# Optimization experiments

Hardware: AMD Instinct MI355X
Metric: run time of the kernel (lower is better)

## Reference

```python
import jax, jax.numpy as jnp
import numpy as np
import math

D_K = 64

def setup_inputs() -> dict:
    key = jax.random.key(0)
    ks = jax.random.split(key, 7)
    B, S, d = 8, 2048, D_K
    H = 4096
    Q = jax.random.normal(ks[0], (B, S, d), dtype=jnp.float32)
    K = jax.random.normal(ks[1], (B, S, d), dtype=jnp.float32)
    V = jax.random.normal(ks[2], (B, S, d), dtype=jnp.float32)
    # Linear params (stored as [in, out]); scaled like torch default init
    W1 = jax.random.normal(ks[3], (S, H), dtype=jnp.float32) / math.sqrt(S)
    b1 = jnp.zeros((H,), dtype=jnp.float32)
    W2 = jax.random.normal(ks[4], (H, S), dtype=jnp.float32) / math.sqrt(H)
    b2 = jnp.zeros((S,), dtype=jnp.float32)
    return {"Q": Q, "K": K, "V": V, "W1": W1, "b1": b1, "W2": W2, "b2": b2}

def reference(Q, K, V, W1, b1, W2, b2):
    # scores: [B, Sq, Sk]
    scores = jnp.einsum('bqd,bkd->bqk', Q, K) / jnp.sqrt(jnp.float32(D_K))
    # 2-layer MLP applied along the last (Sk) axis of the scores
    h = jax.nn.relu(jnp.einsum('bqk,kh->bqh', scores, W1) + b1)
    adjusted = jnp.einsum('bqh,hk->bqk', h, W2) + b2
    attn = jax.nn.softmax(adjusted, axis=-1)
    return jnp.einsum('bqk,bkd->bqd', attn, V)
```

## Files before the change

kernel.cpp:

```cpp
#include <hip/hip_runtime.h>
#include <hip/hip_bf16.h>
#include <stdint.h>

#define S 2048
#define D 64
#define H 4096
#define NB 8

typedef __bf16 bf16;
typedef __attribute__((ext_vector_type(8))) __bf16 bf16x8;
typedef __attribute__((ext_vector_type(4))) __bf16 bf16x4;
typedef __attribute__((ext_vector_type(4))) float f32x4;

__device__ __forceinline__ void dma16_raw(const bf16* g, uint32_t m0_bytes) {
  uint32_t m0s = __builtin_amdgcn_readfirstlane(m0_bytes);
  asm volatile("s_mov_b32 m0, %1\n\t"
               "global_load_lds_dwordx4 %0, off"
               :: "v"(g), "s"(m0s) : "memory");
}

__device__ __forceinline__ uint32_t lds_off_bytes(const void* p) {
  return (uint32_t)(uintptr_t)(__attribute__((address_space(3))) const void*)p;
}

__global__ __launch_bounds__(256) void mega_prep(
    const float* __restrict__ W1, bf16* __restrict__ W1t,
    const float* __restrict__ W2, bf16* __restrict__ W2t,
    const float* __restrict__ Q, bf16* __restrict__ Qb,
    const float* __restrict__ Km, bf16* __restrict__ Kb,
    const float* __restrict__ V, bf16* __restrict__ VtAll) {
  __shared__ float tile[64][65];
  int b = blockIdx.x;
  int tid = threadIdx.x;
  int c4 = (tid & 15) * 4;
  int r16 = tid >> 4;

  if (b < 4096) {
    const float* W; bf16* Wt; int K, N, x, y;
    if (b < 2048) { W = W1; Wt = W1t; K = S; N = H; x = b & 63; y = b >> 6; }
    else { int t = b - 2048; W = W2; Wt = W2t; K = H; N = S; x = t & 31; y = t >> 5; }
    int k0 = y * 64, n0 = x * 64;
#pragma unroll
    for (int i = 0; i < 4; ++i) {
      int r = i * 16 + r16;
      f32x4 v = *(const f32x4*)&W[(size_t)(k0 + r) * N + n0 + c4];
      tile[r][c4 + 0] = v.x; tile[r][c4 + 1] = v.y;
      tile[r][c4 + 2] = v.z; tile[r][c4 + 3] = v.w;
    }
    __syncthreads();
#pragma unroll
    for (int i = 0; i < 4; ++i) {
      int n = i * 16 + r16;
      bf16x4 o;
      o[0] = (bf16)tile[c4 + 0][n]; o[1] = (bf16)tile[c4 + 1][n];
      o[2] = (bf16)tile[c4 + 2][n]; o[3] = (bf16)tile[c4 + 3][n];
      *(bf16x4*)&Wt[(size_t)(n0 + n) * K + k0 + c4] = o;
    }
  } else if (b < 6144) {
    int t = b - 4096;
    const float* x = (t >> 10) ? Km : Q;
    bf16* y = (t >> 10) ? Kb : Qb;
    int i = (t & 1023) * 256 + tid;
    f32x4 v = ((const f32x4*)x)[i];
    bf16x4 o;
    o[0] = (bf16)v.x; o[1] = (bf16)v.y; o[2] = (bf16)v.z; o[3] = (bf16)v.w;
    ((bf16x4*)y)[i] = o;
  } else {
    int t = b - 6144;
    int s0 = (t & 31) * 64;
    int z = t >> 5;
    const float* Vb = V + (size_t)z * (S * D);
    bf16* Vtb = VtAll + (size_t)z * (D * S);
#pragma unroll
    for (int i = 0; i < 4; ++i) {
      int r = i * 16 + r16;
      f32x4 v = *(const f32x4*)&Vb[(size_t)(s0 + r) * D + c4];
      tile[r][c4 + 0] = v.x; tile[r][c4 + 1] = v.y;
      tile[r][c4 + 2] = v.z; tile[r][c4 + 3] = v.w;
    }
    __syncthreads();
#pragma unroll
    for (int i = 0; i < 4; ++i) {
      int n = i * 16 + r16;
      bf16x4 o;
      o[0] = (bf16)tile[c4 + 0][n]; o[1] = (bf16)tile[c4 + 1][n];
      o[2] = (bf16)tile[c4 + 2][n]; o[3] = (bf16)tile[c4 + 3][n];
      *(bf16x4*)&Vtb[(size_t)n * S + s0 + c4] = o;
    }
  }
}

__global__ __launch_bounds__(256) void vt_cast(const float* __restrict__ V,
                                               bf16* __restrict__ Vt) {
  __shared__ float tile[64][65];
  int z = blockIdx.y;
  int s0 = blockIdx.x * 64;
  const float* Vb = V + (size_t)z * (S * D);
  bf16* Vtb = Vt + (size_t)z * (D * S);
  int c4 = (threadIdx.x & 15) * 4;
  int r16 = threadIdx.x >> 4;
#pragma unroll
  for (int i = 0; i < 4; ++i) {
    int r = i * 16 + r16;
    f32x4 v = *(const f32x4*)&Vb[(size_t)(s0 + r) * D + c4];
    tile[r][c4 + 0] = v.x; tile[r][c4 + 1] = v.y;
    tile[r][c4 + 2] = v.z; tile[r][c4 + 3] = v.w;
  }
  __syncthreads();
#pragma unroll
  for (int i = 0; i < 4; ++i) {
    int n = i * 16 + r16;
    bf16x4 o;
    o[0] = (bf16)tile[c4 + 0][n]; o[1] = (bf16)tile[c4 + 1][n];
    o[2] = (bf16)tile[c4 + 2][n]; o[3] = (bf16)tile[c4 + 3][n];
    *(bf16x4*)&Vtb[(size_t)n * S + s0 + c4] = o;
  }
}

__global__ __launch_bounds__(256, 2) void qk_bt(const bf16* __restrict__ Qb,
                                                const bf16* __restrict__ Kb,
                                                bf16* __restrict__ Sc) {
  __shared__ __align__(16) bf16 smem[24576];
  int tid = threadIdx.x;
  int lane = tid & 63;
  int w = tid >> 6;

  int m0 = blockIdx.y * 128, n0 = blockIdx.x * 256;
  const bf16* Ab = Qb + (size_t)blockIdx.z * (S * D);
  const bf16* Btb = Kb + (size_t)blockIdx.z * (S * D);

  int grow = tid >> 2;
  int gcol = (((lane & 3) ^ ((lane >> 3) & 3)) * 8);
  const bf16* gA0 = Ab + (size_t)(m0 + grow) * D + gcol;
  const bf16* gA1 = gA0 + (size_t)64 * D;
  const bf16* gB0 = Btb + (size_t)(n0 + grow) * D + gcol;
  const bf16* gB1 = gB0 + (size_t)64 * D;
  const bf16* gB2 = gB0 + (size_t)128 * D;
  const bf16* gB3 = gB0 + (size_t)192 * D;

  uint32_t ldsBase = lds_off_bytes(&smem[0]);
  uint32_t wb = (uint32_t)(w * 1024);
  uint32_t mA[2], mB[2];
  mA[0] = ldsBase + wb;          mA[1] = ldsBase + 8192 + wb;
  mB[0] = ldsBase + 16384 + wb;  mB[1] = ldsBase + 32768 + wb;

  int mw = (w & 1) * 64, nw = (w >> 1) * 128;
  int lr = lane & 15;
  int ck = lane >> 4;
  int swz = (ck ^ ((lr >> 1) & 3)) * 8;
  const bf16* paBase = smem + (size_t)(mw + lr) * 32 + swz;
  const bf16* pbBase = smem + 8192 + (size_t)(nw + lr) * 32 + swz;

  f32x4 zero = {0.f, 0.f, 0.f, 0.f};
  f32x4 acc[4][8];
#pragma unroll
  for (int mt = 0; mt < 4; ++mt)
#pragma unroll
    for (int nt = 0; nt < 8; ++nt) acc[mt][nt] = zero;

#define STAGE(buf, koff)                                 \
  do {                                                   \
    dma16_raw(gA0 + (koff), mA[buf]);                    \
    dma16_raw(gA1 + (koff), mA[buf] + 4096);             \
    dma16_raw(gB0 + (koff), mB[buf]);                    \
    dma16_raw(gB1 + (koff), mB[buf] + 4096);             \
    dma16_raw(gB2 + (koff), mB[buf] + 8192);             \
    dma16_raw(gB3 + (koff), mB[buf] + 12288);            \
  } while (0)

  STAGE(0, 0);
  STAGE(1, 32);
#undef STAGE

#pragma unroll
  for (int it = 0; it < 2; ++it) {
    if (it == 0)
      asm volatile("s_waitcnt vmcnt(6)\n\ts_barrier" ::: "memory");
    else
      asm volatile("s_waitcnt vmcnt(0)\n\ts_barrier" ::: "memory");
    const bf16* pa = paBase + it * 4096;
    const bf16* pb = pbBase + it * 8192;
    bf16x8 af[4], bfr[8];
#pragma unroll
    for (int mt = 0; mt < 4; ++mt) af[mt] = *(const bf16x8*)(pa + mt * (16 * 32));
#pragma unroll
    for (int nt = 0; nt < 8; ++nt) bfr[nt] = *(const bf16x8*)(pb + nt * (16 * 32));
#pragma unroll
    for (int mt = 0; mt < 4; ++mt)
#pragma unroll
      for (int nt = 0; nt < 8; ++nt)
        acc[mt][nt] = __builtin_amdgcn_mfma_f32_16x16x32_bf16(af[mt], bfr[nt],
                                                              acc[mt][nt], 0, 0, 0);
  }

  bf16* C = Sc + (size_t)blockIdx.z * (S * S);
  int mbase = m0 + mw + (lane >> 4) * 4;
  int nbase = n0 + nw + (lane & 15);
#pragma unroll
  for (int mt = 0; mt < 4; ++mt) {
#pragma unroll
    for (int nt = 0; nt < 8; ++nt) {
      int n = nbase + nt * 16;
#pragma unroll
      for (int reg = 0; reg < 4; ++reg) {
        int m = mbase + mt * 16 + reg;
        C[(size_t)m * S + n] = (bf16)(acc[mt][nt][reg] * 0.125f);
      }
    }
  }
}

template <int RELU, int OUTBF16>
__global__ __launch_bounds__(512, 2) void gemm256(const bf16* __restrict__ A,
                                                  const bf16* __restrict__ Bt,
                                                  const float* __restrict__ bias,
                                                  void* __restrict__ Cv,
                                                  float scale,
                                                  int M, int N, int K,
                                                  long strideA, long strideB,
                                                  long strideC) {
  __shared__ __align__(16) bf16 smem[65536];
  const char* smc = (const char*)&smem[0];

  int tid = threadIdx.x;
  int lane = tid & 63;
  int w = tid >> 6;
  int wm = w >> 2, wn = w & 3;

  unsigned gx = gridDim.x;
  unsigned nwg = gx * gridDim.y;
  unsigned flat = blockIdx.y * gx + blockIdx.x;
  unsigned q = nwg >> 3, r = nwg & 7, xcd = flat & 7, idx = flat >> 3;
  unsigned wg = (xcd < r ? xcd * (q + 1) : r * (q + 1) + (xcd - r) * q) + idx;
  int n0 = (int)(wg % gx) * 256;
  int m0 = (int)(wg / gx) * 256;

  const bf16* Ab = A + (size_t)blockIdx.z * strideA;
  const bf16* Btb = Bt + (size_t)blockIdx.z * strideB;

  int trow = tid >> 3;
  int tg = (tid & 7) ^ (trow & 7);
  const bf16* pgA = Ab + (size_t)(m0 + trow) * K + tg * 8;
  const bf16* pgB = Btb + (size_t)(n0 + trow) * K + tg * 8;
  const size_t s64K = (size_t)K * 64;

  uint32_t ldsBase = lds_off_bytes(&smem[0]);
  uint32_t mb = ldsBase + (uint32_t)(w * 1024);

  int j = lane >> 4, b2 = (lane >> 2) & 1;
  uint32_t rbA0 = (uint32_t)(wm * 8192 + (lane & 15) * 128 +
                             ((j ^ (lane & 3)) * 16) + b2 * 64);
  uint32_t rbA1 = rbA0 ^ 64u;
  uint32_t rbB0 = (uint32_t)(65536 + wn * 4096 + (lane & 15) * 128 +
                             ((j ^ (lane & 3)) * 16) + b2 * 64);
  uint32_t rbB1 = rbB0 ^ 64u;

  f32x4 acc[8][4];
#pragma unroll
  for (int a = 0; a < 8; ++a)
#pragma unroll
    for (int b = 0; b < 2 * 2; ++b) acc[a][b] = (f32x4){0.f, 0.f, 0.f, 0.f};

  bf16x8 af[4][2];
  bf16x8 bf0[2][2];
  bf16x8 bf1[2][2];

#define STG_A(PI, HH, LL, KC) \
  dma16_raw(pgA + (size_t)(2 * (HH) + (LL)) * s64K + (KC), \
            mb + (PI) * 32768 + (HH) * 16384 + (LL) * 8192)
#define STG_B(PI, HH, LL, KC) \
  dma16_raw(pgB + (size_t)(2 * (HH) + (LL)) * s64K + (KC), \
            mb + 65536 + (PI) * 32768 + (HH) * 16384 + (LL) * 8192)
#define STAGE_AH(PI, HH, KC) do { STG_A(PI, HH, 0, KC); STG_A(PI, HH, 1, KC); } while (0)
#define STAGE_BH(PI, HH, KC) do { STG_B(PI, HH, 0, KC); STG_B(PI, HH, 1, KC); } while (0)

#define RDA(PI, QA)                                                            \
  do {                                                                        \
    _Pragma("unroll") for (int mt = 0; mt < 4; ++mt) {                        \
      af[mt][0] = *(const bf16x8*)(smc + rbA0 + ((PI) * 32768 + (QA) * 16384 + mt * 2048)); \
      af[mt][1] = *(const bf16x8*)(smc + rbA1 + ((PI) * 32768 + (QA) * 16384 + mt * 2048)); \
    }                                                                         \
  } while (0)
#define RDB(PI, QB, BF)                                                        \
  do {                                                                        \
    _Pragma("unroll") for (int nt = 0; nt < 2; ++nt) {                        \
      BF[nt][0] = *(const bf16x8*)(smc + rbB0 + ((PI) * 32768 + (QB) * 16384 + nt * 2048)); \
      BF[nt][1] = *(const bf16x8*)(smc + rbB1 + ((PI) * 32768 + (QB) * 16384 + nt * 2048)); \
    }                                                                         \
  } while (0)

#define MFMA_Q(QA, QB, BF)                                                     \
  do {                                                                        \
    __builtin_amdgcn_s_setprio(1);                                            \
    _Pragma("unroll") for (int mt = 0; mt < 4; ++mt)                          \
      _Pragma("unroll") for (int nt = 0; nt < 2; ++nt) {                      \
        f32x4 c = acc[(QA) * 4 + mt][(QB) * 2 + nt];                          \
        c = __builtin_amdgcn_mfma_f32_16x16x32_bf16(af[mt][0], BF[nt][0], c, 0, 0, 0); \
        c = __builtin_amdgcn_mfma_f32_16x16x32_bf16(af[mt][1], BF[nt][1], c, 0, 0, 0); \
        acc[(QA) * 4 + mt][(QB) * 2 + nt] = c;                                \
      }                                                                       \
    __builtin_amdgcn_s_setprio(0);                                            \
  } while (0)

#define BAR() asm volatile("s_barrier" ::: "memory")
#define VMC4() asm volatile("s_waitcnt vmcnt(4)" ::: "memory")

#define TILE2(PI, TT)                                              \
  do {                                                             \
    int c1 = ((TT) + 1 < NT ? (TT) + 1 : NT - 1) * 64;             \
    int c2 = ((TT) + 2 < NT ? (TT) + 2 : NT - 1) * 64;             \
    MFMA_Q(0, 0, bf0);                                             \
    RDB(PI, 1, bf1);                                               \
    STAGE_BH((PI) ^ 1, 0, c1);                                     \
    BAR();                                                         \
    MFMA_Q(0, 1, bf1);                                             \
    RDA(PI, 1);                                                    \
    STAGE_AH(PI, 0, c2);                                           \
    BAR();                                                         \
    STAGE_BH(PI, 1, c2);                                           \
    MFMA_Q(1, 1, bf1);                                             \
    VMC4();                                                        \
    BAR();                                                         \
    MFMA_Q(1, 0, bf0);                                             \
    if ((TT) + 1 < NT) {                                           \
      RDA((PI) ^ 1, 0);                                            \
      RDB((PI) ^ 1, 0, bf0);                                       \
      STAGE_AH(PI, 1, c2);                                         \
      BAR();                                                       \
    }                                                              \
  } while (0)

  STAGE_AH(0, 0, 0);
  STAGE_BH(0, 1, 0);
  STAGE_AH(0, 1, 0);
  STAGE_BH(0, 0, 0);
  STAGE_AH(1, 0, 64);
  STAGE_BH(1, 1, 64);
  asm volatile("s_waitcnt vmcnt(4)\n\ts_barrier" ::: "memory");

  const int NT = K / 64;

  RDA(0, 0);
  RDB(0, 0, bf0);
  STAGE_AH(1, 1, 64);
  BAR();

  for (int T = 0; T < NT; T += 2) {
    TILE2(0, T);
    TILE2(1, T + 1);
  }
#undef TILE2
#undef VMC4
#undef BAR
#undef MFMA_Q
#undef RDB
#undef RDA
#undef STAGE_BH
#undef STAGE_AH
#undef STG_B
#undef STG_A

  asm volatile("s_waitcnt vmcnt(0)" ::: "memory");

  int rowb = m0 + wm * 64 + ((lane >> 4) << 2);
  int colb = n0 + wn * 32 + (lane & 15);
#pragma unroll
  for (int fn = 0; fn < 4; ++fn) {
    int n = colb + (fn >> 1) * 128 + (fn & 1) * 16;
    float bv = bias ? bias[n] : 0.f;
#pragma unroll
    for (int fm = 0; fm < 8; ++fm) {
      int mrow = rowb + (fm >> 2) * 128 + (fm & 3) * 16;
#pragma unroll
      for (int reg = 0; reg < 4; ++reg) {
        float v = acc[fm][fn][reg] * scale + bv;
        if (RELU) v = fmaxf(v, 0.f);
        int m = mrow + reg;
        if (OUTBF16) {
          bf16* C = (bf16*)Cv + (size_t)blockIdx.z * strideC;
          C[(size_t)m * N + n] = (bf16)v;
        } else {
          float* C = (float*)Cv + (size_t)blockIdx.z * strideC;
          C[(size_t)m * N + n] = v;
        }
      }
    }
  }
}

__global__ __launch_bounds__(256) void smav(const float* __restrict__ adj,
                                            const bf16* __restrict__ Vt,
                                            float* __restrict__ out,
                                            long adjStride) {
  int z = blockIdx.y;
  const float* adjb = adj + (size_t)z * adjStride;
  const bf16* Vtb = Vt + (size_t)z * (D * S);
  float* outb = out + (size_t)z * (S * D);
  int q0 = blockIdx.x * 16;
  __shared__ __align__(16) bf16 P[16 * 2048];
  __shared__ float rsum[16];
  int tid = threadIdx.x, w = tid >> 6, lane = tid & 63;
  char* Pc = (char*)&P[0];

#pragma unroll
  for (int i = 0; i < 4; ++i) {
    int r = w * 4 + i;
    const float* rowp = adjb + (size_t)(q0 + r) * S + lane * 4;
    f32x4 rv[8];
    float lm = -1e30f;
#pragma unroll
    for (int kk = 0; kk < 8; ++kk) {
      rv[kk] = *(const f32x4*)(rowp + kk * 256);
      lm = fmaxf(lm, fmaxf(fmaxf(rv[kk].x, rv[kk].y), fmaxf(rv[kk].z, rv[kk].w)));
    }
#pragma unroll
    for (int off = 32; off > 0; off >>= 1) lm = fmaxf(lm, __shfl_xor(lm, off));
    float s = 0.f;
    uint32_t wbase = (uint32_t)(r * 4096 + (lane & 1) * 8);
#pragma unroll
    for (int kk = 0; kk < 8; ++kk) {
      bf16x4 pb;
      pb[0] = (bf16)__expf(rv[kk].x - lm);
      pb[1] = (bf16)__expf(rv[kk].y - lm);
      pb[2] = (bf16)__expf(rv[kk].z - lm);
      pb[3] = (bf16)__expf(rv[kk].w - lm);
      s += (float)pb[0] + (float)pb[1] + (float)pb[2] + (float)pb[3];
      uint32_t g = (uint32_t)(lane >> 1) + (uint32_t)(kk * 32);
      uint32_t gs = g ^ (uint32_t)(r & 7);
      *(bf16x4*)(Pc + wbase + gs * 16) = pb;
    }
#pragma unroll
    for (int off = 32; off > 0; off >>= 1) s += __shfl_xor(s, off);
    if (lane == 0) rsum[r] = s;
  }
  __syncthreads();

  int dl = (w << 4) + (lane & 15);
  const bf16* vrow = Vtb + (size_t)dl * S + (lane >> 4) * 8;
  uint32_t rl = (uint32_t)(lane & 15);
  uint32_t abase = rl * 4096;
  uint32_t rx = rl & 7;
  f32x4 acc0 = {0.f, 0.f, 0.f, 0.f}, acc1 = {0.f, 0.f, 0.f, 0.f};
#pragma unroll 4
  for (int k0 = 0; k0 < S; k0 += 64) {
    uint32_t g0 = (uint32_t)(k0 >> 3) + (uint32_t)(lane >> 4);
    bf16x8 a0 = *(const bf16x8*)(Pc + abase + ((g0 ^ rx) * 16));
    bf16x8 b0 = *(const bf16x8*)(vrow + k0);
    acc0 = __builtin_amdgcn_mfma_f32_16x16x32_bf16(a0, b0, acc0, 0, 0, 0);
    uint32_t g1 = g0 + 4;
    bf16x8 a1 = *(const bf16x8*)(Pc + abase + ((g1 ^ rx) * 16));
    bf16x8 b1 = *(const bf16x8*)(vrow + k0 + 32);
    acc1 = __builtin_amdgcn_mfma_f32_16x16x32_bf16(a1, b1, acc1, 0, 0, 0);
  }
  f32x4 accs = acc0 + acc1;
#pragma unroll
  for (int reg = 0; reg < 4; ++reg) {
    int m = ((lane >> 4) << 2) + reg;
    outb[(size_t)(q0 + m) * D + dl] = accs[reg] / rsum[m];
  }
}

extern "C" void kernel_launch(void* const* d_in, const int* in_sizes, int n_in,
                              void* d_out, int out_size, void* d_ws, size_t ws_size,
                              hipStream_t stream) {
  const float* Q  = (const float*)d_in[0];
  const float* Km = (const float*)d_in[1];
  const float* V  = (const float*)d_in[2];
  const float* W1 = (const float*)d_in[3];
  const float* b1 = (const float*)d_in[4];
  const float* W2 = (const float*)d_in[5];
  const float* b2 = (const float*)d_in[6];
  float* out = (float*)d_out;
  char* ws = (char*)d_ws;

  bf16* W1t  = (bf16*)ws;
  bf16* W2t  = (bf16*)(ws + 16777216);
  bf16* Qb16 = (bf16*)(ws + 33554432);
  bf16* Kb16 = (bf16*)(ws + 35651584);

  int G = 1;
  if (ws_size >= 306184192ULL) G = 8;
  else if (ws_size >= 171966464ULL) G = 4;
  else if (ws_size >= 104857600ULL) G = 2;

  bf16* Sc   = (bf16*)(ws + 37748736);
  float* adj = (float*)(ws + 37748736);
  bf16* h    = (bf16*)(ws + 37748736 + (size_t)G * 16777216);

  size_t vtOff = 37748736ULL + (size_t)G * 33554432ULL;
  bf16* VtAll = nullptr;
  if (ws_size >= vtOff + 2097152ULL) VtAll = (bf16*)(ws + vtOff);

  int prepBlocks = VtAll ? (6144 + NB * 32) : 6144;
  mega_prep<<<dim3(prepBlocks), 256, 0, stream>>>(
      W1, W1t, W2, W2t, Q, Qb16, Km, Kb16, V, VtAll ? VtAll : W1t);

  for (int b0 = 0; b0 < NB; b0 += G) {
    qk_bt<<<dim3(S / 256, S / 128, G), 256, 0, stream>>>(
        Qb16 + (size_t)b0 * S * D, Kb16 + (size_t)b0 * S * D, Sc);
    gemm256<1, 1><<<dim3(H / 256, S / 256, G), 512, 0, stream>>>(
        Sc, W1t, b1, h, 1.0f, S, H, S, (long)S * S, 0L, (long)S * H);
    gemm256<0, 0><<<dim3(S / 256, S / 256, G), 512, 0, stream>>>(
        h, W2t, b2, adj, 1.0f, S, S, H, (long)S * H, 0L, (long)S * S);
    const bf16* VtBase;
    if (VtAll) {
      VtBase = VtAll + (size_t)b0 * D * S;
    } else {
      vt_cast<<<dim3(S / 64, G), 256, 0, stream>>>(V + (size_t)b0 * S * D, h);
      VtBase = h;
    }
    smav<<<dim3(S / 16, G), 256, 0, stream>>>(
        adj, VtBase, out + (size_t)b0 * S * D, (long)S * S);
  }
}
```

Measured before the change: 634.2 us.

## Fuse next group's QK^T into softmax-AV kernel to overlap stages

```diff
diff --git a/kernel.cpp b/kernel.cpp
--- a/kernel.cpp
+++ b/kernel.cpp
@@ -117,17 +117,15 @@
   }
 }
 
-__global__ __launch_bounds__(256, 2) void qk_bt(const bf16* __restrict__ Qb,
-                                                const bf16* __restrict__ Kb,
-                                                bf16* __restrict__ Sc) {
-  __shared__ __align__(16) bf16 smem[24576];
+__device__ __forceinline__ void qk_body(char* smc, const bf16* Ab,
+                                        const bf16* Btb, bf16* C,
+                                        int bx, int by) {
+  bf16* smem = (bf16*)smc;
   int tid = threadIdx.x;
   int lane = tid & 63;
   int w = tid >> 6;
 
-  int m0 = blockIdx.y * 128, n0 = blockIdx.x * 256;
-  const bf16* Ab = Qb + (size_t)blockIdx.z * (S * D);
-  const bf16* Btb = Kb + (size_t)blockIdx.z * (S * D);
+  int m0 = by * 128, n0 = bx * 256;
 
   int grow = tid >> 2;
   int gcol = (((lane & 3) ^ ((lane >> 3) & 3)) * 8);
@@ -138,7 +136,7 @@
   const bf16* gB2 = gB0 + (size_t)128 * D;
   const bf16* gB3 = gB0 + (size_t)192 * D;
 
-  uint32_t ldsBase = lds_off_bytes(&smem[0]);
+  uint32_t ldsBase = lds_off_bytes(smem);
   uint32_t wb = (uint32_t)(w * 1024);
   uint32_t mA[2], mB[2];
   mA[0] = ldsBase + wb;          mA[1] = ldsBase + 8192 + wb;
@@ -158,7 +156,7 @@
 #pragma unroll
     for (int nt = 0; nt < 8; ++nt) acc[mt][nt] = zero;
 
-#define STAGE(buf, koff)                                 \
+#define QK_STAGE(buf, koff)                              \
   do {                                                   \
     dma16_raw(gA0 + (koff), mA[buf]);                    \
     dma16_raw(gA1 + (koff), mA[buf] + 4096);             \
@@ -168,9 +166,9 @@
     dma16_raw(gB3 + (koff), mB[buf] + 12288);            \
   } while (0)
 
-  STAGE(0, 0);
-  STAGE(1, 32);
-#undef STAGE
+  QK_STAGE(0, 0);
+  QK_STAGE(1, 32);
+#undef QK_STAGE
 
 #pragma unroll
   for (int it = 0; it < 2; ++it) {
@@ -193,7 +191,6 @@
                                                               acc[mt][nt], 0, 0, 0);
   }
 
-  bf16* C = Sc + (size_t)blockIdx.z * (S * S);
   int mbase = m0 + mw + (lane >> 4) * 4;
   int nbase = n0 + nw + (lane & 15);
 #pragma unroll
@@ -207,6 +204,97 @@
         C[(size_t)m * S + n] = (bf16)(acc[mt][nt][reg] * 0.125f);
       }
     }
+  }
+}
+
+__device__ __forceinline__ void smav_body(char* u, const float* adjb,
+                                          const bf16* Vtb, float* outb,
+                                          int q0) {
+  char* Pc = u;
+  float* rsum = (float*)(u + 65536);
+  int tid = threadIdx.x, w = tid >> 6, lane = tid & 63;
+
+#pragma unroll
+  for (int i = 0; i < 4; ++i) {
+    int r = w * 4 + i;
+    const float* rowp = adjb + (size_t)(q0 + r) * S + lane * 4;
+    f32x4 rv[8];
+    float lm = -1e30f;
+#pragma unroll
+    for (int kk = 0; kk < 8; ++kk) {
+      rv[kk] = *(const f32x4*)(rowp + kk * 256);
+      lm = fmaxf(lm, fmaxf(fmaxf(rv[kk].x, rv[kk].y), fmaxf(rv[kk].z, rv[kk].w)));
+    }
+#pragma unroll
+    for (int off = 32; off > 0; off >>= 1) lm = fmaxf(lm, __shfl_xor(lm, off));
+    float s = 0.f;
+    uint32_t wbase = (uint32_t)(r * 4096 + (lane & 1) * 8);
+#pragma unroll
+    for (int kk = 0; kk < 8; ++kk) {
+      bf16x4 pb;
+      pb[0] = (bf16)__expf(rv[kk].x - lm);
+      pb[1] = (bf16)__expf(rv[kk].y - lm);
+      pb[2] = (bf16)__expf(rv[kk].z - lm);
+      pb[3] = (bf16)__expf(rv[kk].w - lm);
+      s += (float)pb[0] + (float)pb[1] + (float)pb[2] + (float)pb[3];
+      uint32_t g = (uint32_t)(lane >> 1) + (uint32_t)(kk * 32);
+      uint32_t gs = g ^ (uint32_t)(r & 7);
+      *(bf16x4*)(Pc + wbase + gs * 16) = pb;
+    }
+#pragma unroll
+    for (int off = 32; off > 0; off >>= 1) s += __shfl_xor(s, off);
+    if (lane == 0) rsum[r] = s;
+  }
+  __syncthreads();
+
+  int dl = (w << 4) + (lane & 15);
+  const bf16* vrow = Vtb + (size_t)dl * S + (lane >> 4) * 8;
+  uint32_t rl = (uint32_t)(lane & 15);
+  uint32_t abase = rl * 4096;
+  uint32_t rx = rl & 7;
+  f32x4 acc0 = {0.f, 0.f, 0.f, 0.f}, acc1 = {0.f, 0.f, 0.f, 0.f};
+#pragma unroll 4
+  for (int k0 = 0; k0 < S; k0 += 64) {
+    uint32_t g0 = (uint32_t)(k0 >> 3) + (uint32_t)(lane >> 4);
+    bf16x8 a0 = *(const bf16x8*)(Pc + abase + ((g0 ^ rx) * 16));
+    bf16x8 b0 = *(const bf16x8*)(vrow + k0);
+    acc0 = __builtin_amdgcn_mfma_f32_16x16x32_bf16(a0, b0, acc0, 0, 0, 0);
+    uint32_t g1 = g0 + 4;
+    bf16x8 a1 = *(const bf16x8*)(Pc + abase + ((g1 ^ rx) * 16));
+    bf16x8 b1 = *(const bf16x8*)(vrow + k0 + 32);
+    acc1 = __builtin_amdgcn_mfma_f32_16x16x32_bf16(a1, b1, acc1, 0, 0, 0);
+  }
+  f32x4 accs = acc0 + acc1;
+#pragma unroll
+  for (int reg = 0; reg < 4; ++reg) {
+    int m = ((lane >> 4) << 2) + reg;
+    outb[(size_t)(q0 + m) * D + dl] = accs[reg] / rsum[m];
+  }
+}
+
+__global__ __launch_bounds__(256, 2) void qk_bt(const bf16* __restrict__ Qb,
+                                                const bf16* __restrict__ Kb,
+                                                bf16* __restrict__ Sc) {
+  __shared__ __align__(16) char u[49152];
+  int z = blockIdx.z;
+  qk_body(u, Qb + (size_t)z * (S * D), Kb + (size_t)z * (S * D),
+          Sc + (size_t)z * (S * S), blockIdx.x, blockIdx.y);
+}
+
+__global__ __launch_bounds__(256, 2) void smav_qk(
+    const float* __restrict__ adj, const bf16* __restrict__ Vt,
+    float* __restrict__ out,
+    const bf16* __restrict__ Qbn, const bf16* __restrict__ Kbn,
+    bf16* __restrict__ ScB) {
+  __shared__ __align__(16) char u[65600];
+  int z = blockIdx.y;
+  if (blockIdx.x < 128) {
+    smav_body(u, adj + (size_t)z * (S * S), Vt + (size_t)z * (D * S),
+              out + (size_t)z * (S * D), blockIdx.x * 16);
+  } else {
+    int f = blockIdx.x - 128;
+    qk_body(u, Qbn + (size_t)z * (S * D), Kbn + (size_t)z * (S * D),
+            ScB + (size_t)z * (S * S), f & 7, f >> 3);
   }
 }
 
@@ -388,78 +476,6 @@
   }
 }
 
-__global__ __launch_bounds__(256) void smav(const float* __restrict__ adj,
-                                            const bf16* __restrict__ Vt,
-                                            float* __restrict__ out,
-                                            long adjStride) {
-  int z = blockIdx.y;
-  const float* adjb = adj + (size_t)z * adjStride;
-  const bf16* Vtb = Vt + (size_t)z * (D * S);
-  float* outb = out + (size_t)z * (S * D);
-  int q0 = blockIdx.x * 16;
-  __shared__ __align__(16) bf16 P[16 * 2048];
-  __shared__ float rsum[16];
-  int tid = threadIdx.x, w = tid >> 6, lane = tid & 63;
-  char* Pc = (char*)&P[0];
-
-#pragma unroll
-  for (int i = 0; i < 4; ++i) {
-    int r = w * 4 + i;
-    const float* rowp = adjb + (size_t)(q0 + r) * S + lane * 4;
-    f32x4 rv[8];
-    float lm = -1e30f;
-#pragma unroll
-    for (int kk = 0; kk < 8; ++kk) {
-      rv[kk] = *(const f32x4*)(rowp + kk * 256);
-      lm = fmaxf(lm, fmaxf(fmaxf(rv[kk].x, rv[kk].y), fmaxf(rv[kk].z, rv[kk].w)));
-    }
-#pragma unroll
-    for (int off = 32; off > 0; off >>= 1) lm = fmaxf(lm, __shfl_xor(lm, off));
-    float s = 0.f;
-    uint32_t wbase = (uint32_t)(r * 4096 + (lane & 1) * 8);
-#pragma unroll
-    for (int kk = 0; kk < 8; ++kk) {
-      bf16x4 pb;
-      pb[0] = (bf16)__expf(rv[kk].x - lm);
-      pb[1] = (bf16)__expf(rv[kk].y - lm);
-      pb[2] = (bf16)__expf(rv[kk].z - lm);
-      pb[3] = (bf16)__expf(rv[kk].w - lm);
-      s += (float)pb[0] + (float)pb[1] + (float)pb[2] + (float)pb[3];
-      uint32_t g = (uint32_t)(lane >> 1) + (uint32_t)(kk * 32);
-      uint32_t gs = g ^ (uint32_t)(r & 7);
-      *(bf16x4*)(Pc + wbase + gs * 16) = pb;
-    }
-#pragma unroll
-    for (int off = 32; off > 0; off >>= 1) s += __shfl_xor(s, off);
-    if (lane == 0) rsum[r] = s;
-  }
-  __syncthreads();
-
-  int dl = (w << 4) + (lane & 15);
-  const bf16* vrow = Vtb + (size_t)dl * S + (lane >> 4) * 8;
-  uint32_t rl = (uint32_t)(lane & 15);
-  uint32_t abase = rl * 4096;
-  uint32_t rx = rl & 7;
-  f32x4 acc0 = {0.f, 0.f, 0.f, 0.f}, acc1 = {0.f, 0.f, 0.f, 0.f};
-#pragma unroll 4
-  for (int k0 = 0; k0 < S; k0 += 64) {
-    uint32_t g0 = (uint32_t)(k0 >> 3) + (uint32_t)(lane >> 4);
-    bf16x8 a0 = *(const bf16x8*)(Pc + abase + ((g0 ^ rx) * 16));
-    bf16x8 b0 = *(const bf16x8*)(vrow + k0);
-    acc0 = __builtin_amdgcn_mfma_f32_16x16x32_bf16(a0, b0, acc0, 0, 0, 0);
-    uint32_t g1 = g0 + 4;
-    bf16x8 a1 = *(const bf16x8*)(Pc + abase + ((g1 ^ rx) * 16));
-    bf16x8 b1 = *(const bf16x8*)(vrow + k0 + 32);
-    acc1 = __builtin_amdgcn_mfma_f32_16x16x32_bf16(a1, b1, acc1, 0, 0, 0);
-  }
-  f32x4 accs = acc0 + acc1;
-#pragma unroll
-  for (int reg = 0; reg < 4; ++reg) {
-    int m = ((lane >> 4) << 2) + reg;
-    outb[(size_t)(q0 + m) * D + dl] = accs[reg] / rsum[m];
-  }
-}
-
 extern "C" void kernel_launch(void* const* d_in, const int* in_sizes, int n_in,
                               void* d_out, int out_size, void* d_ws, size_t ws_size,
                               hipStream_t stream) {
@@ -491,25 +507,47 @@
   bf16* VtAll = nullptr;
   if (ws_size >= vtOff + 2097152ULL) VtAll = (bf16*)(ws + vtOff);
 
+  size_t sbOff = vtOff + 2097152ULL;
+  bf16* ScB = nullptr;
+  if (VtAll && ws_size >= sbOff + (size_t)G * 8388608ULL)
+    ScB = (bf16*)(ws + sbOff);
+
   int prepBlocks = VtAll ? (6144 + NB * 32) : 6144;
   mega_prep<<<dim3(prepBlocks), 256, 0, stream>>>(
       W1, W1t, W2, W2t, Q, Qb16, Km, Kb16, V, VtAll ? VtAll : W1t);
 
-  for (int b0 = 0; b0 < NB; b0 += G) {
-    qk_bt<<<dim3(S / 256, S / 128, G), 256, 0, stream>>>(
-        Qb16 + (size_t)b0 * S * D, Kb16 + (size_t)b0 * S * D, Sc);
-    gemm256<1, 1><<<dim3(H / 256, S / 256, G), 512, 0, stream>>>(
-        Sc, W1t, b1, h, 1.0f, S, H, S, (long)S * S, 0L, (long)S * H);
-    gemm256<0, 0><<<dim3(S / 256, S / 256, G), 512, 0, stream>>>(
-        h, W2t, b2, adj, 1.0f, S, S, H, (long)S * H, 0L, (long)S * S);
-    const bf16* VtBase;
-    if (VtAll) {
-      VtBase = VtAll + (size_t)b0 * D * S;
-    } else {
-      vt_cast<<<dim3(S / 64, G), 256, 0, stream>>>(V + (size_t)b0 * S * D, h);
-      VtBase = h;
-    }
-    smav<<<dim3(S / 16, G), 256, 0, stream>>>(
-        adj, VtBase, out + (size_t)b0 * S * D, (long)S * S);
-  }
-}
+  const int ngroups = NB / G;
+  if (ScB) {
+    qk_bt<<<dim3(S / 256, S / 128, G), 256, 0, stream>>>(Qb16, Kb16, ScB);
+    for (int g = 0; g < ngroups; ++g) {
+      int b0 = g * G;
+      gemm256<1, 1><<<dim3(H / 256, S / 256, G), 512, 0, stream>>>(
+          ScB, W1t, b1, h, 1.0f, S, H, S, (long)S * S, 0L, (long)S * H);
+      gemm256<0, 0><<<dim3(S / 256, S / 256, G), 512, 0, stream>>>(
+          h, W2t, b2, adj, 1.0f, S, S, H, (long)S * H, 0L, (long)S * S);
+      int hasNext = (g + 1 < ngroups);
+      int nb0 = (b0 + G) % NB;
+      smav_qk<<<dim3(hasNext ? 256 : 128, G), 256, 0, stream>>>(
+          adj, VtAll + (size_t)b0 * D * S, out + (size_t)b0 * S * D,
+          Qb16 + (size_t)nb0 * S * D, Kb16 + (size_t)nb0 * S * D, ScB);
+    }
+  } else {
+    for (int b0 = 0; b0 < NB; b0 += G) {
+      qk_bt<<<dim3(S / 256, S / 128, G), 256, 0, stream>>>(
+          Qb16 + (size_t)b0 * S * D, Kb16 + (size_t)b0 * S * D, Sc);
+      gemm256<1, 1><<<dim3(H / 256, S / 256, G), 512, 0, stream>>>(
+          Sc, W1t, b1, h, 1.0f, S, H, S, (long)S * S, 0L, (long)S * H);
+      gemm256<0, 0><<<dim3(S / 256, S / 256, G), 512, 0, stream>>>(
+          h, W2t, b2, adj, 1.0f, S, S, H, (long)S * H, 0L, (long)S * S);
+      const bf16* VtBase;
+      if (VtAll) {
+        VtBase = VtAll + (size_t)b0 * D * S;
+      } else {
+        vt_cast<<<dim3(S / 64, G), 256, 0, stream>>>(V + (size_t)b0 * S * D, h);
+        VtBase = h;
+      }
+      smav_qk<<<dim3(128, G), 256, 0, stream>>>(
+          adj, VtBase, out + (size_t)b0 * S * D, Qb16, Kb16, (bf16*)ws);
+    }
+  }
+}
```

Result: faster. 616.7 us (-2.8%).
